# Kernel optimization log

Hardware: AMD Instinct MI355X
Metric: run time of the kernel (lower is better)

Reference implementation:

```python
import jax, jax.numpy as jnp
from jax import lax
import numpy as np

NPOINT, NSAMPLE, RADIUS = 1024, 32, 0.2
BN_EPS = 1e-3  # keras BatchNormalization default epsilon; inference stats: mean=0, var=1


def farthest_point_sample(xyz, npoint):
    # xyz: (B, N, 3) -> (B, npoint) int32, sequential FPS starting at index 0
    def single(pts):
        N = pts.shape[0]
        def body(carry, _):
            dist, far = carry
            d = jnp.sum((pts - pts[far]) ** 2, axis=-1)
            dist = jnp.minimum(dist, d)
            nxt = jnp.argmax(dist).astype(jnp.int32)
            return (dist, nxt), far
        init = (jnp.full((N,), 1e10, pts.dtype), jnp.int32(0))
        _, idx = lax.scan(body, init, None, length=npoint)
        return idx
    return jax.vmap(single)(xyz)


def query_ball_point(radius, nsample, xyz, new_xyz):
    # standard PointNet++ ball query: indices of up to nsample pts within radius,
    # slots with no neighbor filled with the first found index
    B, N, _ = xyz.shape
    sq = (jnp.sum(new_xyz ** 2, -1)[:, :, None]
          + jnp.sum(xyz ** 2, -1)[:, None, :]
          - 2.0 * jnp.einsum('bsd,bnd->bsn', new_xyz, xyz))  # (B, S, N)
    ar = jnp.arange(N, dtype=jnp.int32)
    gidx = jnp.where(sq > radius ** 2, N, ar)
    gidx = jnp.sort(gidx, axis=-1)[..., :nsample]
    first = gidx[..., :1]
    gidx = jnp.where(gidx == N, first, gidx)
    return gidx  # (B, S, nsample)


def group_point(p, idx):
    # p: (B, N, C), idx: (B, S, K) -> (B, S, K, C)
    return jax.vmap(lambda a, i: a[i])(p, idx)


def setup_inputs() -> dict:
    key = jax.random.key(0)
    ks = jax.random.split(key, 8)
    B, N, Cin = 8, 4096, 64
    d = {
        'xyz': jax.random.normal(ks[0], (B, N, 3), dtype=jnp.float32),
        'points': jax.random.normal(ks[1], (B, N, Cin), dtype=jnp.float32),
    }
    chans = [64, 64, 128]
    prev = 3 + Cin
    for i, c in enumerate(chans):
        d[f'W{i}'] = jax.random.normal(ks[2 + i], (prev, c), dtype=jnp.float32) / np.float32(np.sqrt(prev))
        d[f'b{i}'] = jnp.zeros((c,), jnp.float32)
        d[f'g{i}'] = jnp.ones((c,), jnp.float32)
        d[f'beta{i}'] = jnp.zeros((c,), jnp.float32)
        prev = c
    return d


def reference(xyz, points, W0, b0, g0, beta0, W1, b1, g1, beta1, W2, b2, g2, beta2):
    # FPS + gather centroids
    fps_idx = lax.stop_gradient(farthest_point_sample(xyz, NPOINT))  # (B, S)
    new_xyz = jnp.take_along_axis(xyz, fps_idx[..., None], axis=1)   # (B, S, 3)
    # ball query + grouping
    gidx = lax.stop_gradient(query_ball_point(RADIUS, NSAMPLE, xyz, new_xyz))
    grouped_xyz = group_point(xyz, gidx) - new_xyz[:, :, None, :]    # (B, S, K, 3)
    grouped_pts = group_point(points, gidx)                          # (B, S, K, C)
    x = jnp.concatenate([grouped_xyz, grouped_pts], axis=-1)         # (B, S, K, 3+C)
    # shared MLP: Conv2D(c,1,relu) then BatchNorm (inference: mean=0, var=1)
    bn_scale = 1.0 / jnp.sqrt(jnp.float32(1.0) + BN_EPS)
    for W, b, g, be in ((W0, b0, g0, beta0), (W1, b1, g1, beta1), (W2, b2, g2, beta2)):
        x = jax.nn.relu(jnp.einsum('bskc,cd->bskd', x, W) + b)
        x = x * (g * bn_scale) + be
    new_features = jnp.max(x, axis=2)                                # (B, S, C_out)
    return new_xyz, new_features
```

## Files before the change

### kernel.cpp

```cpp
#include <hip/hip_runtime.h>
#include <stdint.h>

#define NB 8
#define NN 4096
#define NP 1024
#define NSAMP 32
#define CIN 64
#define C3 128
#define XS 20
#define SENT_DONE 0x00C0FFEEu
#define GRID1 8

typedef float v2f __attribute__((ext_vector_type(2)));

__device__ __forceinline__ float lo2f(unsigned int u) { return __uint_as_float(u << 16); }
__device__ __forceinline__ float hi2f(unsigned int u) { return __uint_as_float(u & 0xffff0000u); }
__device__ __forceinline__ unsigned short f2b(float f) {
  unsigned int u = __float_as_uint(f);
  unsigned int r = u + 0x7fffu + ((u >> 16) & 1u);
  return (unsigned short)(r >> 16);
}
__device__ __forceinline__ unsigned int packbf(float a, float b) {
  return (unsigned int)f2b(a) | ((unsigned int)f2b(b) << 16);
}

#define FMAXD(v, ctrl)                                                     \
  do {                                                                     \
    int _x = __float_as_int(v);                                            \
    int _m = __builtin_amdgcn_update_dpp(_x, _x, (ctrl), 0xf, 0xf, false); \
    (v) = fmaxf((v), __int_as_float(_m));                                  \
  } while (0)

__global__ __launch_bounds__(1024, 1) void fps_kernel(
    const float* __restrict__ xyz, unsigned short* __restrict__ fps_g,
    float* __restrict__ out_xyz, unsigned int* __restrict__ sent) {
#pragma clang fp contract(off)
  const int tid = threadIdx.x;
  const int b = blockIdx.x;
  const int lane = tid & 63;
  const int wv = tid >> 6;
  __shared__ float sx[NN], sy[NN], sz[NN];
  __shared__ __align__(16) unsigned long long slotmem[2][4];
  __shared__ unsigned short scidx[NP];
  __shared__ unsigned int sdone;
  const float* xb = xyz + (size_t)b * NN * 3;
  if (wv < 4) {
    for (int i = tid; i < NN; i += 256) {
      sx[i] = xb[3 * i + 0];
      sy[i] = xb[3 * i + 1];
      sz[i] = xb[3 * i + 2];
    }
    if (tid < 8) ((unsigned long long*)slotmem)[tid] = 0ull;
    if (tid == 0) { scidx[0] = 0; sdone = 0u; }
  }
  __syncthreads();
  if (wv >= 4) {
#if __has_builtin(__builtin_amdgcn_s_setprio)
    __builtin_amdgcn_s_setprio(0);
#endif
    v2f a[8];
#pragma unroll
    for (int i = 0; i < 8; ++i) {
      float base = 1.0f + (float)(tid & 15) * 1e-6f + (float)i * 1e-7f;
      a[i] = (v2f){base, base + 1e-7f};
    }
    const v2f c1 = (v2f){1.0000001f, 1.0000001f};
    const v2f c2 = (v2f){1e-9f, 1e-9f};
    for (int r = 0; r < 400000; ++r) {
#pragma unroll
      for (int i = 0; i < 8; ++i) a[i] = a[i] * c1 + c2;
      if ((r & 63) == 0) {
        if (__hip_atomic_load(&sdone, __ATOMIC_RELAXED,
                              __HIP_MEMORY_SCOPE_WORKGROUP) != 0u)
          break;
      }
    }
    float s = 0.f;
#pragma unroll
    for (int i = 0; i < 8; ++i) s += a[i].x + a[i].y;
    asm volatile("" ::"v"(s));
  } else {
#if __has_builtin(__builtin_amdgcn_s_setprio)
    __builtin_amdgcn_s_setprio(3);
#endif
    v2f px[8], py[8], pz[8], dd[8];
#pragma unroll
    for (int i = 0; i < 8; ++i) {
      int i0 = tid * 16 + 2 * i;
      px[i] = (v2f){sx[i0], sx[i0 + 1]};
      py[i] = (v2f){sy[i0], sy[i0 + 1]};
      pz[i] = (v2f){sz[i0], sz[i0 + 1]};
      dd[i] = (v2f){1e10f, 1e10f};
    }
    float qx = sx[0], qy = sy[0], qz = sz[0];
    for (int k = 1; k < NP; ++k) {
      v2f q2x = (v2f){qx, qx};
      v2f q2y = (v2f){qy, qy};
      v2f q2z = (v2f){qz, qz};
#pragma unroll
      for (int i = 0; i < 8; ++i) {
        v2f dx = px[i] - q2x;
        v2f dy = py[i] - q2y;
        v2f dz = pz[i] - q2z;
        v2f xx = dx * dx;
        v2f yy = dy * dy;
        v2f zz = dz * dz;
        v2f s = xx + yy;
        v2f d = s + zz;
        dd[i] = __builtin_elementwise_min(dd[i], d);
      }
      float v1[8]; int j1[8];
#pragma unroll
      for (int i = 0; i < 8; ++i) {
        bool g = dd[i].y > dd[i].x;
        v1[i] = g ? dd[i].y : dd[i].x;
        j1[i] = 2 * i + (g ? 1 : 0);
      }
      float v2a[4]; int j2a[4];
#pragma unroll
      for (int i = 0; i < 4; ++i) {
        bool g = v1[2 * i + 1] > v1[2 * i];
        v2a[i] = g ? v1[2 * i + 1] : v1[2 * i];
        j2a[i] = g ? j1[2 * i + 1] : j1[2 * i];
      }
      float v3[2]; int j3[2];
#pragma unroll
      for (int i = 0; i < 2; ++i) {
        bool g = v2a[2 * i + 1] > v2a[2 * i];
        v3[i] = g ? v2a[2 * i + 1] : v2a[2 * i];
        j3[i] = g ? j2a[2 * i + 1] : j2a[2 * i];
      }
      bool g0 = v3[1] > v3[0];
      float bestv = g0 ? v3[1] : v3[0];
      int gi = tid * 16 + (g0 ? j3[1] : j3[0]);
      float m = bestv;
      FMAXD(m, 0x111); FMAXD(m, 0x112); FMAXD(m, 0x114);
      FMAXD(m, 0x118); FMAXD(m, 0x142); FMAXD(m, 0x143);
      float wmax =
          __int_as_float(__builtin_amdgcn_readlane(__float_as_int(m), 63));
      unsigned long long ball = __ballot(bestv == wmax);
      int wl = __ffsll((long long)ball) - 1;
      int widx = __builtin_amdgcn_readlane(gi, wl);
      unsigned long long rec =
          ((unsigned long long)(((unsigned)k << 12) | (unsigned)widx) << 32) |
          (unsigned long long)__float_as_uint(wmax);
      unsigned long long* sl = &slotmem[k & 1][0];
      if (lane == 0) sl[wv] = rec;
      asm volatile("" ::: "memory");
      unsigned long long s0, s1, s2, s3;
      for (;;) {
        ulonglong2 pa = *(const ulonglong2*)(sl);
        ulonglong2 pb = *(const ulonglong2*)(sl + 2);
        s0 = pa.x; s1 = pa.y; s2 = pb.x; s3 = pb.y;
        if ((unsigned)((s0 & s1 & s2 & s3) >> 44) == (unsigned)k) break;
        asm volatile("" ::: "memory");
      }
      float bv = __uint_as_float((unsigned)s0);
      int wi = (int)((s0 >> 32) & 0xFFFu);
      {
        float v = __uint_as_float((unsigned)s1);
        int iw = (int)((s1 >> 32) & 0xFFFu);
        bool g = v > bv; bv = g ? v : bv; wi = g ? iw : wi;
      }
      {
        float v = __uint_as_float((unsigned)s2);
        int iw = (int)((s2 >> 32) & 0xFFFu);
        bool g = v > bv; bv = g ? v : bv; wi = g ? iw : wi;
      }
      {
        float v = __uint_as_float((unsigned)s3);
        int iw = (int)((s3 >> 32) & 0xFFFu);
        bool g = v > bv; bv = g ? v : bv; wi = g ? iw : wi;
      }
      qx = sx[wi]; qy = sy[wi]; qz = sz[wi];
      if (tid == 0) scidx[k] = (unsigned short)wi;
    }
    if (tid == 0)
      __hip_atomic_store(&sdone, 1u, __ATOMIC_RELAXED,
                         __HIP_MEMORY_SCOPE_WORKGROUP);
  }
  __syncthreads();
  for (int i = tid; i < NP; i += 1024) {
    int id = scidx[i];
    out_xyz[((size_t)b * NP + i) * 3 + 0] = sx[id];
    out_xyz[((size_t)b * NP + i) * 3 + 1] = sy[id];
    out_xyz[((size_t)b * NP + i) * 3 + 2] = sz[id];
    fps_g[b * NP + i] = (unsigned short)id;
  }
  __syncthreads();
  if (tid == 0)
    __hip_atomic_store(&sent[b], SENT_DONE, __ATOMIC_RELAXED,
                       __HIP_MEMORY_SCOPE_AGENT);
}

__global__ __launch_bounds__(256) void ballq_kernel(
    const float* __restrict__ xyz, const unsigned short* __restrict__ fps_idx,
    unsigned short* __restrict__ gidx) {
#pragma clang fp contract(off)
  const int tid = threadIdx.x;
  const int gid = blockIdx.x * 4 + (tid >> 6);
  const int lane = tid & 63;
  const int b = gid >> 10;
  const int s = gid & 1023;
  const float* xb = xyz + (size_t)b * NN * 3;
  const int ci = (int)fps_idx[b * NP + s] & (NN - 1);
  const float cx = xb[ci * 3 + 0];
  const float cy = xb[ci * 3 + 1];
  const float cz = xb[ci * 3 + 2];
  const float nn = (cx * cx + cy * cy) + cz * cz;
  const float r2 = 0.04f;
  unsigned short* gout = gidx + (size_t)(b * NP + s) * NSAMP;
  int total = 0;
  int first = -1;
  for (int c = 0; c < NN / 64 && total < NSAMP; ++c) {
    int i = (c << 6) + lane;
    float x = xb[i * 3 + 0];
    float y = xb[i * 3 + 1];
    float z = xb[i * 3 + 2];
    float pp = (x * x + y * y) + z * z;
    float dt = (x * cx + y * cy) + z * cz;
    float sq = (nn + pp) - 2.0f * dt;
    bool inb = !(sq > r2);
    unsigned long long m = __ballot(inb);
    if (first < 0 && m) first = (c << 6) + (__ffsll((unsigned long long)m) - 1);
    int before = __popcll(m & ((1ull << lane) - 1ull));
    int slot = total + before;
    if (inb && slot < NSAMP) gout[slot] = (unsigned short)i;
    total += (int)__popcll(m);
  }
  int cnt = total < NSAMP ? total : NSAMP;
  unsigned short fill = (unsigned short)(first < 0 ? 0 : first);
  if (lane >= cnt && lane < NSAMP) gout[lane] = fill;
}

__global__ __launch_bounds__(256) void mlp_kernel(
    const float* __restrict__ xyz, const float* __restrict__ points,
    const unsigned short* __restrict__ fps_idx, const unsigned short* __restrict__ gidx,
    const float* __restrict__ W0, const float* __restrict__ b0,
    const float* __restrict__ g0, const float* __restrict__ be0,
    const float* __restrict__ W1, const float* __restrict__ b1,
    const float* __restrict__ g1, const float* __restrict__ be1,
    const float* __restrict__ W2, const float* __restrict__ b2,
    const float* __restrict__ g2, const float* __restrict__ be2,
    float* __restrict__ out_feat) {
  __shared__ __align__(16) float wbuf[4352];
  __shared__ __align__(16) unsigned int xpk[8 * 68 * XS];
  __shared__ float prm[768];
  const int tid = threadIdx.x;
  const float bnsc = 1.0f / sqrtf(1.001f);
  if (tid < 64) {
    prm[tid] = b0[tid];       prm[64 + tid] = g0[tid] * bnsc;  prm[128 + tid] = be0[tid];
    prm[192 + tid] = b1[tid]; prm[256 + tid] = g1[tid] * bnsc; prm[320 + tid] = be1[tid];
  }
  if (tid < 128) {
    prm[384 + tid] = b2[tid]; prm[512 + tid] = g2[tid] * bnsc; prm[640 + tid] = be2[tid];
  }
  if (tid < 128) {
    const int cbg = tid >> 4, r2 = tid & 15;
    const int sgg = blockIdx.x * 8 + cbg;
    const int bg = sgg >> 10, sg = sgg & 1023;
    const unsigned short* gi = gidx + (size_t)(bg * NP + sg) * NSAMP;
    const int i0 = (int)gi[2 * r2] & (NN - 1);
    const int i1 = (int)gi[2 * r2 + 1] & (NN - 1);
    const int ci = (int)fps_idx[bg * NP + sg] & (NN - 1);
    const float* xb = xyz + (size_t)bg * NN * 3;
    unsigned int* xc = &xpk[(cbg * 68) * XS + r2];
    const float cx = xb[ci * 3], cy = xb[ci * 3 + 1], cz = xb[ci * 3 + 2];
    xc[0 * XS] = packbf(xb[i0 * 3] - cx,     xb[i1 * 3] - cx);
    xc[1 * XS] = packbf(xb[i0 * 3 + 1] - cy, xb[i1 * 3 + 1] - cy);
    xc[2 * XS] = packbf(xb[i0 * 3 + 2] - cz, xb[i1 * 3 + 2] - cz);
    const float4* p0 = (const float4*)(points + ((size_t)bg * NN + i0) * CIN);
    const float4* p1 = (const float4*)(points + ((size_t)bg * NN + i1) * CIN);
#pragma unroll 4
    for (int kk = 0; kk < 16; ++kk) {
      float4 a = p0[kk], c = p1[kk];
      xc[(3 + 4 * kk) * XS] = packbf(a.x, c.x);
      xc[(4 + 4 * kk) * XS] = packbf(a.y, c.y);
      xc[(5 + 4 * kk) * XS] = packbf(a.z, c.z);
      xc[(6 + 4 * kk) * XS] = packbf(a.w, c.w);
    }
  } else {
    for (int i = tid - 128; i < 67 * 64; i += 128) wbuf[i] = W0[i];
  }
  const int cb = tid >> 5, rg = (tid >> 3) & 3, cg = tid & 7;
  const int sgc = blockIdx.x * 8 + cb;
  const int bc = sgc >> 10, sc = sgc & 1023;
  const unsigned int* xrow = &xpk[(cb * 68) * XS + rg * 4];
  v2f acc2[32];
  auto getacc = [&](int r, int c) -> float {
    v2f t = acc2[r * 4 + (c >> 1)];
    return (c & 1) ? t.y : t.x;
  };
  auto kloop = [&](int K) {
    uint4 xp = *(const uint4*)(xrow);
    float4 wa = *(const float4*)&wbuf[cg * 8];
    float4 wc = *(const float4*)&wbuf[cg * 8 + 4];
#pragma unroll 2
    for (int k = 0; k < K; ++k) {
      uint4 xpn = *(const uint4*)(xrow + (k + 1) * XS);
      float4 wan = *(const float4*)&wbuf[(k + 1) * 64 + cg * 8];
      float4 wcn = *(const float4*)&wbuf[(k + 1) * 64 + cg * 8 + 4];
      float xr[8] = {lo2f(xp.x), hi2f(xp.x), lo2f(xp.y), hi2f(xp.y),
                     lo2f(xp.z), hi2f(xp.z), lo2f(xp.w), hi2f(xp.w)};
      v2f w01 = (v2f){wa.x, wa.y};
      v2f w23 = (v2f){wa.z, wa.w};
      v2f w45 = (v2f){wc.x, wc.y};
      v2f w67 = (v2f){wc.z, wc.w};
#pragma unroll
      for (int r = 0; r < 8; ++r) {
        v2f xq = (v2f){xr[r], xr[r]};
        acc2[r * 4 + 0] = __builtin_elementwise_fma(xq, w01, acc2[r * 4 + 0]);
        acc2[r * 4 + 1] = __builtin_elementwise_fma(xq, w23, acc2[r * 4 + 1]);
        acc2[r * 4 + 2] = __builtin_elementwise_fma(xq, w45, acc2[r * 4 + 2]);
        acc2[r * 4 + 3] = __builtin_elementwise_fma(xq, w67, acc2[r * 4 + 3]);
      }
      xp = xpn; wa = wan; wc = wcn;
    }
  };
  auto hwrite = [&](int pofs) {
#pragma unroll
    for (int c = 0; c < 8; ++c) {
      int cl = cg * 8 + c;
      float bia = prm[pofs + cl], gg = prm[pofs + 64 + cl], bb = prm[pofs + 128 + cl];
      unsigned int* hc = &xpk[(cb * 68 + cl) * XS + rg * 4];
#pragma unroll
      for (int i = 0; i < 4; ++i) {
        float za = getacc(2 * i, c) + bia;
        za = za > 0.f ? za : 0.f;
        za = za * gg + bb;
        float zb = getacc(2 * i + 1, c) + bia;
        zb = zb > 0.f ? zb : 0.f;
        zb = zb * gg + bb;
        hc[i] = packbf(za, zb);
      }
    }
  };
  __syncthreads();
#pragma unroll
  for (int i = 0; i < 32; ++i) acc2[i] = (v2f){0.f, 0.f};
  kloop(67);
  __syncthreads();
  hwrite(0);
  for (int i = tid; i < 64 * 64; i += 256) wbuf[i] = W1[i];
  __syncthreads();
#pragma unroll
  for (int i = 0; i < 32; ++i) acc2[i] = (v2f){0.f, 0.f};
  kloop(64);
  __syncthreads();
  hwrite(192);
  for (int i = tid; i < 64 * 64; i += 256) wbuf[i] = W2[(i >> 6) * C3 + (i & 63)];
  __syncthreads();
  float* outp = out_feat + (size_t)(bc * NP + sc) * C3;
#pragma unroll 1
  for (int half = 0; half < 2; ++half) {
    if (half) {
      __syncthreads();
      for (int i = tid; i < 64 * 64; i += 256)
        wbuf[i] = W2[(i >> 6) * C3 + 64 + (i & 63)];
      __syncthreads();
    }
#pragma unroll
    for (int i = 0; i < 32; ++i) acc2[i] = (v2f){0.f, 0.f};
    kloop(64);
    float vout[8];
#pragma unroll
    for (int c = 0; c < 8; ++c) {
      int cl = half * 64 + cg * 8 + c;
      float bia = prm[384 + cl], gg = prm[512 + cl], bb = prm[640 + cl];
      float mmax = -3.4e38f;
#pragma unroll
      for (int r = 0; r < 8; ++r) {
        float z = getacc(r, c) + bia;
        z = z > 0.f ? z : 0.f;
        z = z * gg + bb;
        mmax = fmaxf(mmax, z);
      }
      mmax = fmaxf(mmax, __shfl_xor(mmax, 8, 64));
      mmax = fmaxf(mmax, __shfl_xor(mmax, 16, 64));
      vout[c] = mmax;
    }
    if (rg == 0) {
      *(float4*)(outp + half * 64 + cg * 8) =
          make_float4(vout[0], vout[1], vout[2], vout[3]);
      *(float4*)(outp + half * 64 + cg * 8 + 4) =
          make_float4(vout[4], vout[5], vout[6], vout[7]);
    }
  }
}

extern "C" void kernel_launch(void* const* d_in, const int* in_sizes, int n_in,
                              void* d_out, int out_size, void* d_ws, size_t ws_size,
                              hipStream_t stream) {
  const float* xyz = (const float*)d_in[0];
  const float* points = (const float*)d_in[1];
  const float* W0 = (const float*)d_in[2];
  const float* b0 = (const float*)d_in[3];
  const float* g0 = (const float*)d_in[4];
  const float* be0 = (const float*)d_in[5];
  const float* W1 = (const float*)d_in[6];
  const float* b1 = (const float*)d_in[7];
  const float* g1 = (const float*)d_in[8];
  const float* be1 = (const float*)d_in[9];
  const float* W2 = (const float*)d_in[10];
  const float* b2 = (const float*)d_in[11];
  const float* g2 = (const float*)d_in[12];
  const float* be2 = (const float*)d_in[13];
  float* out = (float*)d_out;
  unsigned short* fps = (unsigned short*)d_ws;
  unsigned short* gidx = fps + (size_t)NB * NP;
  unsigned int* sent = (unsigned int*)((char*)d_ws + (16 + 512) * 1024);
  hipMemsetAsync(sent, 0, NB * sizeof(unsigned int), stream);
  fps_kernel<<<GRID1, 1024, 0, stream>>>(xyz, fps, out, sent);
  ballq_kernel<<<(NB * NP) / 4, 256, 0, stream>>>(xyz, fps, gidx);
  mlp_kernel<<<NB * NP / 8, 256, 0, stream>>>(xyz, points, fps, gidx,
                                              W0, b0, g0, be0, W1, b1, g1, be1,
                                              W2, b2, g2, be2,
                                              out + (size_t)NB * NP * 3);
}
```

Before: 853.8 us.

## Fuse ball query into MLP kernel via shared-memory neighbor indices

Removes the separate ball-query kernel and runs the query inside the MLP kernel: each wave computes neighbor indices for two centroids and writes them to shared memory, which the gather stage then reads. This drops one kernel launch and the global write and read of the index array. In exchange the MLP blocks do the serial radius scan before their gather, which adds latency per block, and the kernel uses a little more shared memory.

```diff
diff --git a/kernel.cpp b/kernel.cpp
--- a/kernel.cpp
+++ b/kernel.cpp
@@ -193,49 +193,9 @@
                        __HIP_MEMORY_SCOPE_AGENT);
 }
 
-__global__ __launch_bounds__(256) void ballq_kernel(
-    const float* __restrict__ xyz, const unsigned short* __restrict__ fps_idx,
-    unsigned short* __restrict__ gidx) {
-#pragma clang fp contract(off)
-  const int tid = threadIdx.x;
-  const int gid = blockIdx.x * 4 + (tid >> 6);
-  const int lane = tid & 63;
-  const int b = gid >> 10;
-  const int s = gid & 1023;
-  const float* xb = xyz + (size_t)b * NN * 3;
-  const int ci = (int)fps_idx[b * NP + s] & (NN - 1);
-  const float cx = xb[ci * 3 + 0];
-  const float cy = xb[ci * 3 + 1];
-  const float cz = xb[ci * 3 + 2];
-  const float nn = (cx * cx + cy * cy) + cz * cz;
-  const float r2 = 0.04f;
-  unsigned short* gout = gidx + (size_t)(b * NP + s) * NSAMP;
-  int total = 0;
-  int first = -1;
-  for (int c = 0; c < NN / 64 && total < NSAMP; ++c) {
-    int i = (c << 6) + lane;
-    float x = xb[i * 3 + 0];
-    float y = xb[i * 3 + 1];
-    float z = xb[i * 3 + 2];
-    float pp = (x * x + y * y) + z * z;
-    float dt = (x * cx + y * cy) + z * cz;
-    float sq = (nn + pp) - 2.0f * dt;
-    bool inb = !(sq > r2);
-    unsigned long long m = __ballot(inb);
-    if (first < 0 && m) first = (c << 6) + (__ffsll((unsigned long long)m) - 1);
-    int before = __popcll(m & ((1ull << lane) - 1ull));
-    int slot = total + before;
-    if (inb && slot < NSAMP) gout[slot] = (unsigned short)i;
-    total += (int)__popcll(m);
-  }
-  int cnt = total < NSAMP ? total : NSAMP;
-  unsigned short fill = (unsigned short)(first < 0 ? 0 : first);
-  if (lane >= cnt && lane < NSAMP) gout[lane] = fill;
-}
-
 __global__ __launch_bounds__(256) void mlp_kernel(
     const float* __restrict__ xyz, const float* __restrict__ points,
-    const unsigned short* __restrict__ fps_idx, const unsigned short* __restrict__ gidx,
+    const unsigned short* __restrict__ fps_idx,
     const float* __restrict__ W0, const float* __restrict__ b0,
     const float* __restrict__ g0, const float* __restrict__ be0,
     const float* __restrict__ W1, const float* __restrict__ b1,
@@ -246,6 +206,7 @@
   __shared__ __align__(16) float wbuf[4352];
   __shared__ __align__(16) unsigned int xpk[8 * 68 * XS];
   __shared__ float prm[768];
+  __shared__ unsigned short sgi[8][NSAMP];
   const int tid = threadIdx.x;
   const float bnsc = 1.0f / sqrtf(1.001f);
   if (tid < 64) {
@@ -255,13 +216,53 @@
   if (tid < 128) {
     prm[384 + tid] = b2[tid]; prm[512 + tid] = g2[tid] * bnsc; prm[640 + tid] = be2[tid];
   }
+  {
+#pragma clang fp contract(off)
+    const int wv2 = tid >> 6;
+    const int lane = tid & 63;
+#pragma unroll 1
+    for (int j = 0; j < 2; ++j) {
+      const int cw = wv2 * 2 + j;
+      const int sgq = blockIdx.x * 8 + cw;
+      const int bq = sgq >> 10, sq = sgq & 1023;
+      const float* xbq = xyz + (size_t)bq * NN * 3;
+      const int ci = (int)fps_idx[bq * NP + sq] & (NN - 1);
+      const float cx = xbq[ci * 3 + 0];
+      const float cy = xbq[ci * 3 + 1];
+      const float cz = xbq[ci * 3 + 2];
+      const float nn = (cx * cx + cy * cy) + cz * cz;
+      const float r2 = 0.04f;
+      int total = 0;
+      int first = -1;
+      for (int c = 0; c < NN / 64 && total < NSAMP; ++c) {
+        int i = (c << 6) + lane;
+        float x = xbq[i * 3 + 0];
+        float y = xbq[i * 3 + 1];
+        float z = xbq[i * 3 + 2];
+        float pp = (x * x + y * y) + z * z;
+        float dt = (x * cx + y * cy) + z * cz;
+        float sq2 = (nn + pp) - 2.0f * dt;
+        bool inb = !(sq2 > r2);
+        unsigned long long m = __ballot(inb);
+        if (first < 0 && m)
+          first = (c << 6) + (__ffsll((unsigned long long)m) - 1);
+        int before = __popcll(m & ((1ull << lane) - 1ull));
+        int slot = total + before;
+        if (inb && slot < NSAMP) sgi[cw][slot] = (unsigned short)i;
+        total += (int)__popcll(m);
+      }
+      int cnt = total < NSAMP ? total : NSAMP;
+      unsigned short fill = (unsigned short)(first < 0 ? 0 : first);
+      if (lane >= cnt && lane < NSAMP) sgi[cw][lane] = fill;
+    }
+  }
+  __syncthreads();
   if (tid < 128) {
     const int cbg = tid >> 4, r2 = tid & 15;
     const int sgg = blockIdx.x * 8 + cbg;
     const int bg = sgg >> 10, sg = sgg & 1023;
-    const unsigned short* gi = gidx + (size_t)(bg * NP + sg) * NSAMP;
-    const int i0 = (int)gi[2 * r2] & (NN - 1);
-    const int i1 = (int)gi[2 * r2 + 1] & (NN - 1);
+    const int i0 = (int)sgi[cbg][2 * r2] & (NN - 1);
+    const int i1 = (int)sgi[cbg][2 * r2 + 1] & (NN - 1);
     const int ci = (int)fps_idx[bg * NP + sg] & (NN - 1);
     const float* xb = xyz + (size_t)bg * NN * 3;
     unsigned int* xc = &xpk[(cbg * 68) * XS + r2];
@@ -407,12 +408,10 @@
   const float* be2 = (const float*)d_in[13];
   float* out = (float*)d_out;
   unsigned short* fps = (unsigned short*)d_ws;
-  unsigned short* gidx = fps + (size_t)NB * NP;
   unsigned int* sent = (unsigned int*)((char*)d_ws + (16 + 512) * 1024);
   hipMemsetAsync(sent, 0, NB * sizeof(unsigned int), stream);
   fps_kernel<<<GRID1, 1024, 0, stream>>>(xyz, fps, out, sent);
-  ballq_kernel<<<(NB * NP) / 4, 256, 0, stream>>>(xyz, fps, gidx);
-  mlp_kernel<<<NB * NP / 8, 256, 0, stream>>>(xyz, points, fps, gidx,
+  mlp_kernel<<<NB * NP / 8, 256, 0, stream>>>(xyz, points, fps,
                                               W0, b0, g0, be0, W1, b1, g1, be1,
                                               W2, b2, g2, be2,
                                               out + (size_t)NB * NP * 3);
```

After: 894.0 us. 1.05x slower.
